# Performance work log

Hardware: AMD Instinct MI355X
Metric: run time of the kernel (lower is better)

Reference implementation:

```python
import jax, jax.numpy as jnp
import numpy as np

VOCAB = 50000
WORD_EMB = 300
N_QNODE = 3
N_KNODE = 3
HID = 512
N_OUT = 300
N_ANS = 32000
N_LAYERS = 3
MIN_NORM = 1e-15
EPS = 1e-7

# ---- Hyperboloid manifold ops (HGCN convention, curvature c, K = 1/c) ----

def proj_tan0(u):
    # zero out the time coordinate
    return u.at[..., :1].set(0.0)

def expmap0(u, c):
    K = 1.0 / c
    sqrtK = jnp.sqrt(K)
    d = u[..., 1:]
    n = jnp.clip(jnp.linalg.norm(d, axis=-1, keepdims=True), MIN_NORM, None)
    theta = n / sqrtK
    return jnp.concatenate([sqrtK * jnp.cosh(theta), sqrtK * jnp.sinh(theta) * d / n], axis=-1)

def logmap0(x, c):
    K = 1.0 / c
    sqrtK = jnp.sqrt(K)
    d = x[..., 1:]
    n = jnp.clip(jnp.linalg.norm(d, axis=-1, keepdims=True), MIN_NORM, None)
    theta = jnp.clip(x[..., :1] / sqrtK, 1.0 + EPS, None)
    rest = sqrtK * jnp.arccosh(theta) * d / n
    return jnp.concatenate([jnp.zeros_like(rest[..., :1]), rest], axis=-1)

def proj(x, c):
    K = 1.0 / c
    d = x[..., 1:]
    first = jnp.sqrt(jnp.clip(K + jnp.sum(d * d, axis=-1, keepdims=True), EPS, None))
    return jnp.concatenate([first, d], axis=-1)

def hyperbolic_emb(x, c):
    return proj(expmap0(proj_tan0(x), c), c)


def setup_inputs() -> dict:
    key = jax.random.key(0)
    ks = jax.random.split(key, 16)
    B, NQ, NK = 256, 30, 100
    inp = {}
    inp['he_ques_id'] = jax.random.randint(ks[0], (B, NQ, N_QNODE), 0, VOCAB)
    inp['he_kg_id'] = jax.random.randint(ks[1], (B, NK, N_KNODE), 0, VOCAB)
    inp['emb_table'] = jax.random.normal(ks[2], (VOCAB, WORD_EMB), jnp.float32)
    inp['q2h_w'] = jax.random.normal(ks[3], (WORD_EMB * N_QNODE, HID), jnp.float32) * 0.01
    inp['q2h_b'] = jnp.zeros((HID,), jnp.float32)
    inp['k2h_w'] = jax.random.normal(ks[4], (WORD_EMB * N_KNODE, HID), jnp.float32) * 0.01
    inp['k2h_b'] = jnp.zeros((HID,), jnp.float32)
    inp['Wk'] = jax.random.normal(ks[5], (N_LAYERS, HID, HID), jnp.float32) * 0.05
    inp['Wq'] = jax.random.normal(ks[6], (N_LAYERS, HID, HID), jnp.float32) * 0.05
    inp['curv'] = jnp.ones((N_LAYERS + 1,), jnp.float32)
    inp['proj1_w'] = jax.random.normal(ks[7], (2 * HID, HID), jnp.float32) * 0.02
    inp['proj1_b'] = jnp.zeros((HID,), jnp.float32)
    inp['proj2_w'] = jax.random.normal(ks[8], (HID, N_OUT), jnp.float32) * 0.02
    inp['proj2_b'] = jnp.zeros((N_OUT,), jnp.float32)
    inp['glove_cands'] = jax.random.normal(ks[9], (N_ANS, N_OUT), jnp.float32)
    return inp


def reference(he_ques_id, he_kg_id, emb_table, q2h_w, q2h_b, k2h_w, k2h_b,
              Wk, Wq, curv, proj1_w, proj1_b, proj2_w, proj2_b, glove_cands):
    B = he_ques_id.shape[0]
    c0 = curv[0]
    cL = curv[N_LAYERS]

    # embedding lookup + flatten hyperedge nodes
    he_q = emb_table[he_ques_id].reshape(B, he_ques_id.shape[1], -1)  # (B,Nq,900)
    he_k = emb_table[he_kg_id].reshape(B, he_kg_id.shape[1], -1)      # (B,Nk,900)
    he_q = jnp.where(jnp.isnan(he_q), 0.0, he_q)
    he_k = jnp.where(jnp.isnan(he_k), 0.0, he_k)

    he_q = he_q @ q2h_w + q2h_b   # (B,Nq,H)
    he_k = he_k @ k2h_w + k2h_b   # (B,Nk,H)

    q = hyperbolic_emb(he_q, c0)  # (B,Nq,H) on hyperboloid
    k = hyperbolic_emb(he_k, c0)  # (B,Nk,H)

    scale = 1.0 / np.sqrt(HID)
    for i in range(N_LAYERS):
        c_in, c_out = curv[i], curv[i + 1]
        kt = proj_tan0(logmap0(k, c_in))
        qt = proj_tan0(logmap0(q, c_in))
        kp = kt @ Wk[i]
        qp = qt @ Wq[i]
        s = jnp.einsum('bkh,bqh->bkq', kp, qp) * scale
        att_k = jnp.einsum('bkq,bqh->bkh', jax.nn.softmax(s, axis=-1), qt) + kt
        att_q = jnp.einsum('bqk,bkh->bqh', jax.nn.softmax(jnp.swapaxes(s, 1, 2), axis=-1), kt) + qt
        k = proj(expmap0(proj_tan0(att_k), c_out), c_out)
        q = proj(expmap0(proj_tan0(att_q), c_out), c_out)

    # mean pool over hyperedges, concat kg||ques
    last_kq = jnp.concatenate([k.mean(axis=1), q.mean(axis=1)], axis=1)  # (B,2H)
    euc = proj_tan0(logmap0(last_kq, cL))
    h = jax.nn.relu(euc @ proj1_w + proj1_b)
    out = h @ proj2_w + proj2_b               # (B,300)
    sim = out @ glove_cands.T                 # (B,32000)
    pred = jax.nn.log_softmax(sim, axis=1)
    return pred
```

## Files before the change

### kernel.cpp

```cpp
#include <hip/hip_runtime.h>
#include <math.h>

#define BATCH 256
#define NQ 30
#define NK 100
#define HID 512
#define WORD 300
#define KIN 900
#define KP 928
#define NANS 32000
#define NOUT 300
#define NOUTP 384
#define NTG 12
#define NLAYERS 3
#define MQT (BATCH * NQ)
#define MKT (BATCH * NK)
#define SCALE 0.044194173824159216f
#define KTLD 520
#define CLDST 136

typedef __attribute__((ext_vector_type(8))) short bf16x8;
typedef __attribute__((ext_vector_type(4))) float f32x4;
typedef unsigned short ushort_t;

__device__ __forceinline__ unsigned short f2bf(float f) {
  unsigned int u = __float_as_uint(f);
  u = (u + 0x7FFF + ((u >> 16) & 1)) >> 16;
  return (unsigned short)u;
}
__device__ __forceinline__ float bf2f(unsigned short s) {
  return __uint_as_float(((unsigned int)s) << 16);
}

typedef const __attribute__((address_space(1))) unsigned int* gas_u32;
typedef __attribute__((address_space(3))) unsigned int* las_u32;
__device__ __forceinline__ void gld_lds16(const void* g, void* l) {
  __builtin_amdgcn_global_load_lds((gas_u32)g, (las_u32)l, 16, 0, 0);
}

__device__ __forceinline__ int xcd_swz_linear() {
  const int nwg = gridDim.x * gridDim.y;
  const int orig = blockIdx.y * gridDim.x + blockIdx.x;
  const int q = nwg >> 3, r = nwg & 7;
  const int xcd = orig & 7, idx = orig >> 3;
  return (xcd < r ? xcd * (q + 1) : r * (q + 1) + (xcd - r) * q) + idx;
}

__device__ __forceinline__ float waveReduceSum(float v) {
#pragma unroll
  for (int o = 32; o > 0; o >>= 1) v += __shfl_xor(v, o);
  return v;
}
__device__ float blockReduceSum512(float v) {
  __shared__ float sm[8];
  int lane = threadIdx.x & 63, w = threadIdx.x >> 6;
  v = waveReduceSum(v);
  if (lane == 0) sm[w] = v;
  __syncthreads();
  float r = 0.f;
#pragma unroll
  for (int i = 0; i < 8; ++i) r += sm[i];
  __syncthreads();
  return r;
}

template <int SWZB, int BIAS, int OUTF32, int OUTBF16, int ZC0, int RELU>
__global__ __launch_bounds__(256) void mfma_gemm2(
    const ushort_t* __restrict__ A1, const ushort_t* __restrict__ Bt1,
    const float* __restrict__ bias1, float* __restrict__ C1,
    ushort_t* __restrict__ Cb1, int M1b,
    const ushort_t* __restrict__ A2, const ushort_t* __restrict__ Bt2,
    const float* __restrict__ bias2, float* __restrict__ C2,
    ushort_t* __restrict__ Cb2,
    size_t zsA, size_t zsB, size_t zsC,
    int N, int K, int nbias) {
  __shared__ __align__(16) ushort_t smem[128 * CLDST];
  const int wg = xcd_swz_linear();
  const int bx = wg % gridDim.x, by = wg / gridDim.x;
  const int z = blockIdx.z;
  const bool sel = (by >= M1b);
  const ushort_t* A = (sel ? A2 : A1) + z * zsA;
  const ushort_t* Bt = (sel ? Bt2 : Bt1) + z * zsB;
  const float* bias = sel ? bias2 : bias1;
  float* C = (sel ? C2 : C1);
  ushort_t* Cb = (sel ? Cb2 : Cb1);
  if (C) C += z * zsC;
  if (Cb) Cb += z * zsC;
  const int row0 = (sel ? (by - M1b) : by) * 128;
  const int col0 = bx * 128;

  const int tid = threadIdx.x;
  const int lane = tid & 63, w = tid >> 6;
  const int wr = w >> 1, wc = w & 1;
  const int s_r = lane & 15, s_kq = lane >> 4;
  const int nt = K / 32;

  const size_t a_src0 = (size_t)(row0 + (w * 2 + 0) * 16 + s_r) * K + s_kq * 8;
  const size_t a_src1 = (size_t)(row0 + (w * 2 + 1) * 16 + s_r) * K + s_kq * 8;
  const size_t b_lin0 = (size_t)(col0 + (w * 2 + 0) * 16 + s_r) * K + s_kq * 8;
  const size_t b_lin1 = (size_t)(col0 + (w * 2 + 1) * 16 + s_r) * K + s_kq * 8;
  const size_t b_swz0 = ((size_t)(col0 >> 7) * nt) * 4096 + (w * 2 + 0) * 512 + lane * 8;
  const size_t b_swz1 = b_swz0 + 512;

  auto stageAB = [&](int t, int bsel) {
    const int k0 = t * 32;
    ushort_t* Ab = smem + bsel * 4096;
    ushort_t* Bb = smem + 8192 + bsel * 4096;
    gld_lds16(A + a_src0 + k0, Ab + (w * 2 + 0) * 512);
    gld_lds16(A + a_src1 + k0, Ab + (w * 2 + 1) * 512);
    if (SWZB) {
      gld_lds16(Bt + b_swz0 + (size_t)t * 4096, Bb + (w * 2 + 0) * 512);
      gld_lds16(Bt + b_swz1 + (size_t)t * 4096, Bb + (w * 2 + 1) * 512);
    } else {
      gld_lds16(Bt + b_lin0 + k0, Bb + (w * 2 + 0) * 512);
      gld_lds16(Bt + b_lin1 + k0, Bb + (w * 2 + 1) * 512);
    }
  };

  f32x4 acc[4][4];
#pragma unroll
  for (int i = 0; i < 4; ++i)
#pragma unroll
    for (int j = 0; j < 4; ++j) acc[i][j] = (f32x4){0.f, 0.f, 0.f, 0.f};

  stageAB(0, 0);
  __syncthreads();
  for (int t = 0; t < nt; ++t) {
    const int cur = t & 1;
    if (t + 1 < nt) stageAB(t + 1, cur ^ 1);
    const ushort_t* Ab = smem + cur * 4096;
    const ushort_t* Bb = smem + 8192 + cur * 4096;
    bf16x8 af[4], bfr[4];
#pragma unroll
    for (int mi = 0; mi < 4; ++mi)
      af[mi] = *(const bf16x8*)(Ab + (wr * 4 + mi) * 512 + lane * 8);
#pragma unroll
    for (int nj = 0; nj < 4; ++nj)
      bfr[nj] = *(const bf16x8*)(Bb + (wc * 4 + nj) * 512 + lane * 8);
#pragma unroll
    for (int mi = 0; mi < 4; ++mi)
#pragma unroll
      for (int nj = 0; nj < 4; ++nj)
        acc[mi][nj] = __builtin_amdgcn_mfma_f32_16x16x32_bf16(
            af[mi], bfr[nj], acc[mi][nj], 0, 0, 0);
    __syncthreads();
  }

  if (OUTBF16) {
#pragma unroll
    for (int nj = 0; nj < 4; ++nj) {
      const int nl = wc * 64 + nj * 16 + (lane & 15);
      const int n = col0 + nl;
      const float bb = BIAS ? ((n < nbias) ? bias[n] : 0.f) : 0.f;
#pragma unroll
      for (int mi = 0; mi < 4; ++mi) {
        f32x4 v = acc[mi][nj];
#pragma unroll
        for (int r = 0; r < 4; ++r) {
          const int ml = wr * 64 + mi * 16 + (lane >> 4) * 4 + r;
          float val = v[r] + bb;
          if (RELU) val = fmaxf(val, 0.f);
          if (ZC0 && n == 0) val = 0.f;
          smem[ml * CLDST + nl] = f2bf(val);
        }
      }
    }
    __syncthreads();
#pragma unroll
    for (int j = 0; j < 8; ++j) {
      const int e = j * 2048 + tid * 8;
      const int ml = e >> 7, nl = e & 127;
      uint4 v = *(const uint4*)(smem + ml * CLDST + nl);
      *(uint4*)(Cb + (size_t)(row0 + ml) * N + col0 + nl) = v;
    }
  }
  if (OUTF32) {
#pragma unroll
    for (int nj = 0; nj < 4; ++nj) {
      const int n = col0 + wc * 64 + nj * 16 + (lane & 15);
      const float bb = BIAS ? ((n < nbias) ? bias[n] : 0.f) : 0.f;
#pragma unroll
      for (int mi = 0; mi < 4; ++mi) {
        f32x4 v = acc[mi][nj];
#pragma unroll
        for (int r = 0; r < 4; ++r) {
          const int m = row0 + wr * 64 + mi * 16 + (lane >> 4) * 4 + r;
          float val = v[r] + bb;
          if (RELU) val = fmaxf(val, 0.f);
          if (ZC0 && n == 0) val = 0.f;
          C[(size_t)m * N + n] = val;
        }
      }
    }
  }
}

__global__ __launch_bounds__(256) void gather_all_k(
    const int* __restrict__ qid, const int* __restrict__ kid,
    const float* __restrict__ emb, ushort_t* __restrict__ gq,
    ushort_t* __restrict__ gk) {
  int m = blockIdx.x;
  const int* ids;
  ushort_t* outp;
  if (m < MQT) {
    ids = qid + m * 3;
    outp = gq + (size_t)m * KP;
  } else {
    m -= MQT;
    ids = kid + m * 3;
    outp = gk + (size_t)m * KP;
  }
  const int t = threadIdx.x;
  if (t >= KP / 4) return;
  const int k = t * 4;
  ushort4 o = make_ushort4(0, 0, 0, 0);
  if (k < KIN) {
    const int node = (k >= 600) ? 2 : ((k >= 300) ? 1 : 0);
    const int off = k - node * 300;
    const int id = ids[node];
    float4 v = *(const float4*)(emb + (size_t)id * 300 + off);
    if (v.x != v.x) v.x = 0.f;
    if (v.y != v.y) v.y = 0.f;
    if (v.z != v.z) v.z = 0.f;
    if (v.w != v.w) v.w = 0.f;
    o = make_ushort4(f2bf(v.x), f2bf(v.y), f2bf(v.z), f2bf(v.w));
  }
  *(ushort4*)(outp + k) = o;
}

__global__ __launch_bounds__(256) void tcast4_k(
    const float* __restrict__ q2h_w, const float* __restrict__ k2h_w,
    const float* __restrict__ p1w, const float* __restrict__ p2w,
    ushort_t* __restrict__ q2h_wt, ushort_t* __restrict__ k2h_wt,
    ushort_t* __restrict__ p1wt, ushort_t* __restrict__ p2wt) {
  const int z = blockIdx.z;
  const float* src;
  ushort_t* dst;
  int R, Cc, Rp, Cp;
  if (z == 0)      { src = q2h_w; dst = q2h_wt; R = KIN;  Cc = HID;  Rp = KP;   Cp = HID; }
  else if (z == 1) { src = k2h_w; dst = k2h_wt; R = KIN;  Cc = HID;  Rp = KP;   Cp = HID; }
  else if (z == 2) { src = p1w; dst = p1wt; R = 1024; Cc = HID;  Rp = 1024; Cp = HID; }
  else             { src = p2w; dst = p2wt; R = HID;  Cc = NOUT; Rp = HID;  Cp = NOUTP; }
  const int r0 = blockIdx.y * 32, c0 = blockIdx.x * 32;
  if (r0 >= Rp || c0 >= Cp) return;
  __shared__ float t[32][33];
  const int tx = threadIdx.x & 31, ty = threadIdx.x >> 5;
#pragma unroll
  for (int i = 0; i < 4; ++i) {
    int r = r0 + ty + i * 8, c = c0 + tx;
    t[ty + i * 8][tx] = (r < R && c < Cc) ? src[(size_t)r * Cc + c] : 0.f;
  }
  __syncthreads();
#pragma unroll
  for (int i = 0; i < 4; ++i) {
    int c = c0 + ty + i * 8, r = r0 + tx;
    if (c < Cp && r < Rp) dst[(size_t)c * Rp + r] = f2bf(t[tx][ty + i * 8]);
  }
}

__global__ __launch_bounds__(256) void gcast_swz_k(
    const float* __restrict__ glove, ushort_t* __restrict__ gs) {
  const int ts = blockIdx.x, gp = blockIdx.y;
  ushort_t* dst = gs + ((size_t)gp * NTG + ts) * 4096;
  for (int g = threadIdx.x; g < 512; g += 256) {
    const int o = g * 8;
    const int chunk = o >> 9, kq = (o >> 7) & 3, rl = (o >> 3) & 15;
    const int row = gp * 128 + chunk * 16 + rl;
    const int kb = ts * 32 + kq * 8;
    ushort_t tmp[8];
    if (kb + 8 <= NOUT) {
      const float* s = glove + (size_t)row * NOUT + kb;
      float2 a0 = *(const float2*)(s + 0);
      float2 a1 = *(const float2*)(s + 2);
      float2 a2 = *(const float2*)(s + 4);
      float2 a3 = *(const float2*)(s + 6);
      tmp[0] = f2bf(a0.x); tmp[1] = f2bf(a0.y);
      tmp[2] = f2bf(a1.x); tmp[3] = f2bf(a1.y);
      tmp[4] = f2bf(a2.x); tmp[5] = f2bf(a2.y);
      tmp[6] = f2bf(a3.x); tmp[7] = f2bf(a3.y);
    } else {
#pragma unroll
      for (int j = 0; j < 8; ++j) {
        const int k = kb + j;
        tmp[j] = (k < NOUT) ? f2bf(glove[(size_t)row * NOUT + k]) : (ushort_t)0;
      }
    }
    *(ushort4*)(dst + o) = make_ushort4(tmp[0], tmp[1], tmp[2], tmp[3]);
    *(ushort4*)(dst + o + 4) = make_ushort4(tmp[4], tmp[5], tmp[6], tmp[7]);
  }
}

__global__ __launch_bounds__(128) void castrows_k(
    const float* __restrict__ Wk, const float* __restrict__ Wq,
    ushort_t* __restrict__ Wkr, ushort_t* __restrict__ Wqr) {
  const int idx = blockIdx.x;
  const int mat = idx >> 9, row = idx & 511;
  const float* src = (mat < 3 ? Wk + (size_t)mat * HID * HID
                              : Wq + (size_t)(mat - 3) * HID * HID) + (size_t)row * HID;
  ushort_t* dst = (mat < 3 ? Wkr + (size_t)mat * HID * HID
                           : Wqr + (size_t)(mat - 3) * HID * HID) + (size_t)row * HID;
  const int k = threadIdx.x * 4;
  float4 v = *(const float4*)(src + k);
  *(ushort4*)(dst + k) = make_ushort4(f2bf(v.x), f2bf(v.y), f2bf(v.z), f2bf(v.w));
}

__global__ __launch_bounds__(512) void att_fused_k(
    const ushort_t* __restrict__ Qp, const ushort_t* __restrict__ Ktc,
    const ushort_t* __restrict__ Qc, ushort_t* __restrict__ Kn,
    ushort_t* __restrict__ Qn) {
  const int b = blockIdx.x;
  __shared__ float S_lds[NK][32];
  __shared__ float PqT[NK][32];
  __shared__ __align__(16) ushort_t kts[NK * KTLD];
  __shared__ __align__(16) ushort_t qts[NQ * HID];
  const int tid = threadIdx.x;
  const int w = tid >> 6, lane = tid & 63;
  const ushort_t* ktg = Ktc + (size_t)b * NK * HID;
  const ushort_t* qtg = Qc + (size_t)b * NQ * HID;

  for (int e = tid; e < NK * 64; e += 512) {
    const int r = e >> 6, c16 = e & 63;
    gld_lds16(ktg + (size_t)r * HID + c16 * 8, kts + (size_t)r * KTLD + c16 * 8);
  }
  for (int e = tid; e < NQ * 64; e += 512) {
    const int r = e >> 6, c16 = e & 63;
    gld_lds16(qtg + (size_t)r * HID + c16 * 8, qts + (size_t)r * HID + c16 * 8);
  }
  __syncthreads();

  if (w < 7) {
    const int r = lane & 15, kq = lane >> 4;
    const ushort_t* qpb = Qp + (size_t)b * NQ * HID;
    const int rowA = w * 16 + r;
    const int rowA_c = (rowA < NK) ? rowA : (NK - 1);
    const int qr1 = (16 + r) < NQ ? (16 + r) : NQ - 1;
    f32x4 a0 = {0.f, 0.f, 0.f, 0.f}, a1 = {0.f, 0.f, 0.f, 0.f};
    for (int k0 = 0; k0 < HID; k0 += 32) {
      bf16x8 af = *(const bf16x8*)(kts + (size_t)rowA_c * KTLD + k0 + kq * 8);
      bf16x8 b0 = *(const bf16x8*)(qpb + (size_t)r * HID + k0 + kq * 8);
      bf16x8 b1 = *(const bf16x8*)(qpb + (size_t)qr1 * HID + k0 + kq * 8);
      a0 = __builtin_amdgcn_mfma_f32_16x16x32_bf16(af, b0, a0, 0, 0, 0);
      a1 = __builtin_amdgcn_mfma_f32_16x16x32_bf16(af, b1, a1, 0, 0, 0);
    }
    const int q0 = lane & 15, mb = (lane >> 4) * 4;
#pragma unroll
    for (int rr = 0; rr < 4; ++rr) {
      const int mA = w * 16 + mb + rr;
      if (mA < NK) {
        S_lds[mA][q0] = a0[rr] * SCALE;
        if (q0 + 16 < NQ) S_lds[mA][q0 + 16] = a1[rr] * SCALE;
      }
    }
  }
  __syncthreads();
  if (tid < NQ) {
    const int q = tid;
    float m = -1e30f;
    for (int kr = 0; kr < NK; ++kr) m = fmaxf(m, S_lds[kr][q]);
    float s = 0.f;
    for (int kr = 0; kr < NK; ++kr) {
      float e = expf(S_lds[kr][q] - m);
      PqT[kr][q] = e;
      s += e;
    }
    float inv = 1.f / s;
    for (int kr = 0; kr < NK; ++kr) PqT[kr][q] *= inv;
  } else if (tid >= 32 && tid < 32 + NK) {
    const int kr = tid - 32;
    PqT[kr][30] = 0.f;
    PqT[kr][31] = 0.f;
  }
  __syncthreads();
  if (tid < NK) {
    const int kr = tid;
    float m = -1e30f;
#pragma unroll
    for (int q = 0; q < NQ; ++q) m = fmaxf(m, S_lds[kr][q]);
    float s = 0.f;
    float e[NQ];
#pragma unroll
    for (int q = 0; q < NQ; ++q) {
      e[q] = expf(S_lds[kr][q] - m);
      s += e[q];
    }
    float inv = 1.f / s;
#pragma unroll
    for (int q = 0; q < NQ; ++q) S_lds[kr][q] = e[q] * inv;
    S_lds[kr][30] = 0.f;
    S_lds[kr][31] = 0.f;
  }
  __syncthreads();

  const int c = tid;
  float qx[32], ax[32];
#pragma unroll
  for (int q = 0; q < NQ; ++q) qx[q] = bf2f(qts[q * HID + c]);
  qx[30] = 0.f;
  qx[31] = 0.f;
#pragma unroll
  for (int i = 0; i < 32; ++i) ax[i] = 0.f;
  ushort_t* kout = Kn + (size_t)b * NK * HID;
  for (int kr = 0; kr < NK; ++kr) {
    const float kx = bf2f(kts[(size_t)kr * KTLD + c]);
    float sx = kx;
#pragma unroll
    for (int g = 0; g < 8; ++g) {
      float4 pk = *(const float4*)&S_lds[kr][g * 4];
      sx = fmaf(pk.x, qx[g * 4 + 0], sx);
      sx = fmaf(pk.y, qx[g * 4 + 1], sx);
      sx = fmaf(pk.z, qx[g * 4 + 2], sx);
      sx = fmaf(pk.w, qx[g * 4 + 3], sx);
      float4 pq = *(const float4*)&PqT[kr][g * 4];
      ax[g * 4 + 0] = fmaf(pq.x, kx, ax[g * 4 + 0]);
      ax[g * 4 + 1] = fmaf(pq.y, kx, ax[g * 4 + 1]);
      ax[g * 4 + 2] = fmaf(pq.z, kx, ax[g * 4 + 2]);
      ax[g * 4 + 3] = fmaf(pq.w, kx, ax[g * 4 + 3]);
    }
    kout[(size_t)kr * HID + c] = f2bf(sx);
  }
  ushort_t* qout = Qn + (size_t)b * NQ * HID;
#pragma unroll
  for (int q = 0; q < NQ; ++q)
    qout[(size_t)q * HID + c] = f2bf(ax[q] + qx[q]);
}

__global__ __launch_bounds__(512) void finale_k(
    const ushort_t* __restrict__ Kb, const ushort_t* __restrict__ Qb,
    ushort_t* __restrict__ lastb, const float* __restrict__ curv) {
  const int b = blockIdx.x, tid = threadIdx.x;
  const int w = tid >> 6, lane = tid & 63;
  const float c = curv[NLAYERS];
  const float Kc = 1.f / c, sqrtK = sqrtf(Kc);
  __shared__ float fsc[NK + NQ];
  __shared__ float fst[NK + NQ];
  const ushort_t* xkp = Kb + (size_t)b * NK * HID;
  const ushort_t* xqp = Qb + (size_t)b * NQ * HID;

  for (int r = w; r < NK + NQ; r += 8) {
    const ushort_t* row =
        (r < NK) ? (xkp + (size_t)r * HID) : (xqp + (size_t)(r - NK) * HID);
    bf16x8 v = *(const bf16x8*)(row + lane * 8);
    float ss = 0.f;
#pragma unroll
    for (int j = 0; j < 8; ++j) {
      float t = bf2f((unsigned short)v[j]);
      ss = fmaf(t, t, ss);
    }
    ss = waveReduceSum(ss);
    if (lane == 0) {
      float n = fmaxf(sqrtf(ss), 1e-15f);
      float f = sqrtK * sinhf(n / sqrtK) / n;
      fsc[r] = f;
      fst[r] = sqrtf(fmaxf(Kc + f * f * ss, 1e-7f));
    }
  }
  __syncthreads();

  float mk, mq;
  if (tid == 0) {
    float sk = 0.f, sq2 = 0.f;
    for (int r = 0; r < NK; ++r) sk += fst[r];
    for (int r = 0; r < NQ; ++r) sq2 += fst[NK + r];
    mk = sk;
    mq = sq2;
  } else {
    float sk = 0.f, sq2 = 0.f;
    for (int r = 0; r < NK; ++r)
      sk = fmaf(fsc[r], bf2f(xkp[(size_t)r * HID + tid]), sk);
    for (int r = 0; r < NQ; ++r)
      sq2 = fmaf(fsc[NK + r], bf2f(xqp[(size_t)r * HID + tid]), sq2);
    mk = sk;
    mq = sq2;
  }
  mk *= (1.f / NK);
  mq *= (1.f / NQ);

  float sq = ((tid == 0) ? 0.f : mk * mk) + mq * mq;
  float ssall = blockReduceSum512(sq);
  __shared__ float x0sh;
  if (tid == 0) x0sh = mk;
  __syncthreads();
  const float x0 = x0sh;
  const float n = fmaxf(sqrtf(ssall), 1e-15f);
  const float theta = fmaxf(x0 / sqrtK, 1.f + 1e-7f);
  const float rr = sqrtK * acoshf(theta) / n;
  ushort_t* ob = lastb + (size_t)b * 1024;
  ob[tid] = (tid == 0) ? (ushort_t)0 : f2bf(rr * mk);
  ob[512 + tid] = f2bf(rr * mq);
}

__global__ __launch_bounds__(512) void logsoftmax_k(float* __restrict__ x) {
  const int b = blockIdx.x, tid = threadIdx.x;
  float4* row = (float4*)(x + (size_t)b * NANS);
  float m = -3.4e38f, s = 0.f;
  for (int i = tid; i < NANS / 4; i += 512) {
    float4 v = row[i];
    float lm = fmaxf(fmaxf(v.x, v.y), fmaxf(v.z, v.w));
    float nm = fmaxf(m, lm);
    s = s * expf(m - nm) + expf(v.x - nm) + expf(v.y - nm) +
        expf(v.z - nm) + expf(v.w - nm);
    m = nm;
  }
#pragma unroll
  for (int o = 32; o > 0; o >>= 1) {
    float mo = __shfl_xor(m, o);
    float so = __shfl_xor(s, o);
    float nm = fmaxf(m, mo);
    s = s * expf(m - nm) + so * expf(mo - nm);
    m = nm;
  }
  __shared__ float smm[8], sms[8];
  const int w = tid >> 6, lane = tid & 63;
  if (lane == 0) { smm[w] = m; sms[w] = s; }
  __syncthreads();
  float gm = smm[0], gs = sms[0];
#pragma unroll
  for (int i = 1; i < 8; ++i) {
    float nm = fmaxf(gm, smm[i]);
    gs = gs * expf(gm - nm) + sms[i] * expf(smm[i] - nm);
    gm = nm;
  }
  const float lse = gm + logf(gs);
  for (int i = tid; i < NANS / 4; i += 512) {
    float4 v = row[i];
    v.x -= lse; v.y -= lse; v.z -= lse; v.w -= lse;
    row[i] = v;
  }
}

extern "C" void kernel_launch(void* const* d_in, const int* in_sizes, int n_in,
                              void* d_out, int out_size, void* d_ws, size_t ws_size,
                              hipStream_t stream) {
  const int* qid = (const int*)d_in[0];
  const int* kid = (const int*)d_in[1];
  const float* emb = (const float*)d_in[2];
  const float* q2h_w = (const float*)d_in[3];
  const float* q2h_b = (const float*)d_in[4];
  const float* k2h_w = (const float*)d_in[5];
  const float* k2h_b = (const float*)d_in[6];
  const float* Wk = (const float*)d_in[7];
  const float* Wq = (const float*)d_in[8];
  const float* curv = (const float*)d_in[9];
  const float* p1w = (const float*)d_in[10];
  const float* p1b = (const float*)d_in[11];
  const float* p2w = (const float*)d_in[12];
  const float* p2b = (const float*)d_in[13];
  const float* glove = (const float*)d_in[14];
  float* out = (float*)d_out;

  ushort_t* u = (ushort_t*)d_ws;
  ushort_t* Ks0 = u;
  ushort_t* Ks1 = Ks0 + (size_t)MKT * HID;
  ushort_t* Qs0 = Ks1 + (size_t)MKT * HID;
  ushort_t* Qs1 = Qs0 + (size_t)MQT * HID;
  ushort_t* Qps = Qs1 + (size_t)MQT * HID;
  ushort_t* gq = Qps + (size_t)MQT * HID;
  ushort_t* gk = gq + (size_t)MQT * KP;
  ushort_t* q2h_wt = gk + (size_t)MKT * KP;
  ushort_t* k2h_wt = q2h_wt + (size_t)HID * KP;
  ushort_t* Wkr = k2h_wt + (size_t)HID * KP;
  ushort_t* Wqr = Wkr + (size_t)NLAYERS * HID * HID;
  ushort_t* Mb = Wqr + (size_t)NLAYERS * HID * HID;
  ushort_t* p1wt = Mb + (size_t)NLAYERS * HID * HID;
  ushort_t* p2wt = p1wt + (size_t)HID * 1024;
  ushort_t* lastb = p2wt + (size_t)NOUTP * HID;
  ushort_t* h1b = lastb + (size_t)BATCH * 1024;
  ushort_t* o2b = h1b + (size_t)BATCH * HID;
  ushort_t* gsw = o2b + (size_t)BATCH * NOUTP;

  gather_all_k<<<MQT + MKT, 256, 0, stream>>>(qid, kid, emb, gq, gk);
  tcast4_k<<<dim3(16, 32, 4), 256, 0, stream>>>(
      q2h_w, k2h_w, p1w, p2w, q2h_wt, k2h_wt, p1wt, p2wt);
  castrows_k<<<6 * HID, 128, 0, stream>>>(Wk, Wq, Wkr, Wqr);
  gcast_swz_k<<<dim3(NTG, 250), 256, 0, stream>>>(glove, gsw);

  mfma_gemm2<0, 0, 0, 1, 0, 0><<<dim3(HID / 128, HID / 128, NLAYERS), 256, 0, stream>>>(
      Wkr, Wqr, nullptr, nullptr, Mb, HID / 128,
      Wkr, Wqr, nullptr, nullptr, Mb,
      (size_t)HID * HID, (size_t)HID * HID, (size_t)HID * HID, HID, HID, HID);

  mfma_gemm2<0, 1, 0, 1, 1, 0><<<dim3(HID / 128, MQT / 128 + MKT / 128), 256, 0, stream>>>(
      gq, q2h_wt, q2h_b, nullptr, Qs0, MQT / 128,
      gk, k2h_wt, k2h_b, nullptr, Ks0, 0, 0, 0, HID, KP, HID);

  ushort_t* Kc = Ks0;
  ushort_t* Kn = Ks1;
  ushort_t* Qc = Qs0;
  ushort_t* Qn = Qs1;
  for (int i = 0; i < NLAYERS; ++i) {
    mfma_gemm2<0, 0, 0, 1, 0, 0><<<dim3(HID / 128, MQT / 128), 256, 0, stream>>>(
        Qc, Mb + (size_t)i * HID * HID, nullptr, nullptr, Qps, MQT / 128,
        Qc, Mb + (size_t)i * HID * HID, nullptr, nullptr, Qps,
        0, 0, 0, HID, HID, HID);
    att_fused_k<<<BATCH, 512, 0, stream>>>(Qps, Kc, Qc, Kn, Qn);
    ushort_t* t1 = Kc; Kc = Kn; Kn = t1;
    ushort_t* t2 = Qc; Qc = Qn; Qn = t2;
  }

  finale_k<<<BATCH, 512, 0, stream>>>(Kc, Qc, lastb, curv);

  mfma_gemm2<0, 1, 0, 1, 0, 1><<<dim3(HID / 128, BATCH / 128), 256, 0, stream>>>(
      lastb, p1wt, p1b, nullptr, h1b, BATCH / 128,
      lastb, p1wt, p1b, nullptr, h1b, 0, 0, 0, HID, 1024, HID);
  mfma_gemm2<0, 1, 0, 1, 0, 0><<<dim3(NOUTP / 128, BATCH / 128), 256, 0, stream>>>(
      h1b, p2wt, p2b, nullptr, o2b, BATCH / 128,
      h1b, p2wt, p2b, nullptr, o2b, 0, 0, 0, NOUTP, HID, NOUT);
  mfma_gemm2<1, 0, 1, 0, 0, 0><<<dim3(NANS / 128, BATCH / 128), 256, 0, stream>>>(
      o2b, gsw, nullptr, out, nullptr, BATCH / 128,
      o2b, gsw, nullptr, out, nullptr, 0, 0, 0, NANS, NOUTP, NANS);
  logsoftmax_k<<<BATCH, 512, 0, stream>>>(out);
}
```

Before: 445.9 us.

## Compute attention-weighted aggregations in att_fused_k with bf16 MFMA

Replaces the per-thread scalar FMA loops for the two attention products (P_k·Q and P_q^T·K) with 16x16x32 bf16 MFMA tiles. Softmax probabilities are now stored as bf16 in LDS, padded to K=32 or 128, and the S buffer gets a padded stride. The goal is to move the per-column scalar work and register-heavy accumulators onto matrix cores. In exchange it adds bf16 rounding of the probabilities, gathers of strided 2-byte elements from LDS to build the B fragments, and scattered 2-byte global stores.

```diff
diff --git a/kernel.cpp b/kernel.cpp
--- a/kernel.cpp
+++ b/kernel.cpp
@@ -18,6 +18,8 @@
 #define SCALE 0.044194173824159216f
 #define KTLD 520
 #define CLDST 136
+#define SST 36
+#define PQLD 136
 
 typedef __attribute__((ext_vector_type(8))) short bf16x8;
 typedef __attribute__((ext_vector_type(4))) float f32x4;
@@ -309,8 +311,8 @@
     const ushort_t* __restrict__ Qc, ushort_t* __restrict__ Kn,
     ushort_t* __restrict__ Qn) {
   const int b = blockIdx.x;
-  __shared__ float S_lds[NK][32];
-  __shared__ float PqT[NK][32];
+  __shared__ __align__(16) float S_lds[112 * SST];
+  __shared__ __align__(16) ushort_t Pq[32 * PQLD];
   __shared__ __align__(16) ushort_t kts[NK * KTLD];
   __shared__ __align__(16) ushort_t qts[NQ * HID];
   const int tid = threadIdx.x;
@@ -347,81 +349,133 @@
     for (int rr = 0; rr < 4; ++rr) {
       const int mA = w * 16 + mb + rr;
       if (mA < NK) {
-        S_lds[mA][q0] = a0[rr] * SCALE;
-        if (q0 + 16 < NQ) S_lds[mA][q0 + 16] = a1[rr] * SCALE;
-      }
-    }
-  }
-  __syncthreads();
+        S_lds[mA * SST + q0] = a0[rr] * SCALE;
+        if (q0 + 16 < NQ) S_lds[mA * SST + q0 + 16] = a1[rr] * SCALE;
+      }
+    }
+  }
+  __syncthreads();
+  float e2[NQ];
+  float inv2 = 0.f;
+  const int kr2 = tid - 32;
+  const bool do2b = (kr2 >= 0 && kr2 < NK);
   if (tid < NQ) {
     const int q = tid;
     float m = -1e30f;
-    for (int kr = 0; kr < NK; ++kr) m = fmaxf(m, S_lds[kr][q]);
+    for (int kr = 0; kr < NK; ++kr) m = fmaxf(m, S_lds[kr * SST + q]);
     float s = 0.f;
-    for (int kr = 0; kr < NK; ++kr) {
-      float e = expf(S_lds[kr][q] - m);
-      PqT[kr][q] = e;
-      s += e;
-    }
+    for (int kr = 0; kr < NK; ++kr) s += expf(S_lds[kr * SST + q] - m);
     float inv = 1.f / s;
-    for (int kr = 0; kr < NK; ++kr) PqT[kr][q] *= inv;
-  } else if (tid >= 32 && tid < 32 + NK) {
-    const int kr = tid - 32;
-    PqT[kr][30] = 0.f;
-    PqT[kr][31] = 0.f;
-  }
-  __syncthreads();
-  if (tid < NK) {
-    const int kr = tid;
+    for (int kr = 0; kr < NK; ++kr)
+      Pq[q * PQLD + kr] = f2bf(expf(S_lds[kr * SST + q] - m) * inv);
+    for (int kr = NK; kr < 128; ++kr) Pq[q * PQLD + kr] = 0;
+  } else if (tid < 32) {
+    for (int kr = 0; kr < 128; ++kr) Pq[tid * PQLD + kr] = 0;
+  } else if (do2b) {
     float m = -1e30f;
 #pragma unroll
-    for (int q = 0; q < NQ; ++q) m = fmaxf(m, S_lds[kr][q]);
+    for (int q = 0; q < NQ; ++q) m = fmaxf(m, S_lds[kr2 * SST + q]);
     float s = 0.f;
-    float e[NQ];
 #pragma unroll
     for (int q = 0; q < NQ; ++q) {
-      e[q] = expf(S_lds[kr][q] - m);
-      s += e[q];
-    }
-    float inv = 1.f / s;
-#pragma unroll
-    for (int q = 0; q < NQ; ++q) S_lds[kr][q] = e[q] * inv;
-    S_lds[kr][30] = 0.f;
-    S_lds[kr][31] = 0.f;
-  }
-  __syncthreads();
-
-  const int c = tid;
-  float qx[32], ax[32];
-#pragma unroll
-  for (int q = 0; q < NQ; ++q) qx[q] = bf2f(qts[q * HID + c]);
-  qx[30] = 0.f;
-  qx[31] = 0.f;
-#pragma unroll
-  for (int i = 0; i < 32; ++i) ax[i] = 0.f;
-  ushort_t* kout = Kn + (size_t)b * NK * HID;
-  for (int kr = 0; kr < NK; ++kr) {
-    const float kx = bf2f(kts[(size_t)kr * KTLD + c]);
-    float sx = kx;
-#pragma unroll
-    for (int g = 0; g < 8; ++g) {
-      float4 pk = *(const float4*)&S_lds[kr][g * 4];
-      sx = fmaf(pk.x, qx[g * 4 + 0], sx);
-      sx = fmaf(pk.y, qx[g * 4 + 1], sx);
-      sx = fmaf(pk.z, qx[g * 4 + 2], sx);
-      sx = fmaf(pk.w, qx[g * 4 + 3], sx);
-      float4 pq = *(const float4*)&PqT[kr][g * 4];
-      ax[g * 4 + 0] = fmaf(pq.x, kx, ax[g * 4 + 0]);
-      ax[g * 4 + 1] = fmaf(pq.y, kx, ax[g * 4 + 1]);
-      ax[g * 4 + 2] = fmaf(pq.z, kx, ax[g * 4 + 2]);
-      ax[g * 4 + 3] = fmaf(pq.w, kx, ax[g * 4 + 3]);
-    }
-    kout[(size_t)kr * HID + c] = f2bf(sx);
-  }
-  ushort_t* qout = Qn + (size_t)b * NQ * HID;
-#pragma unroll
-  for (int q = 0; q < NQ; ++q)
-    qout[(size_t)q * HID + c] = f2bf(ax[q] + qx[q]);
+      e2[q] = expf(S_lds[kr2 * SST + q] - m);
+      s += e2[q];
+    }
+    inv2 = 1.f / s;
+  }
+  __syncthreads();
+  ushort_t* Pk = (ushort_t*)S_lds;
+  if (do2b) {
+    ushort_t* prow = Pk + kr2 * 72;
+#pragma unroll
+    for (int q = 0; q < NQ; ++q) prow[q] = f2bf(e2[q] * inv2);
+    prow[30] = 0;
+    prow[31] = 0;
+  }
+  __syncthreads();
+
+  const int cl = lane & 15, g8 = (lane >> 4) * 8;
+  {
+    bf16x8 bk[4];
+#pragma unroll
+    for (int nt = 0; nt < 4; ++nt) {
+      const int col = w * 64 + nt * 16 + cl;
+      union { ushort_t u[8]; bf16x8 v; } pb;
+#pragma unroll
+      for (int j = 0; j < 8; ++j) {
+        const int q = g8 + j;
+        pb.u[j] = qts[(q < NQ ? q : NQ - 1) * HID + col];
+      }
+      bk[nt] = pb.v;
+    }
+    ushort_t* kout = Kn + (size_t)b * NK * HID;
+#pragma unroll
+    for (int mt = 0; mt < 7; ++mt) {
+      bf16x8 af = *(const bf16x8*)(Pk + (mt * 16 + cl) * 72 + g8);
+      f32x4 ac[4];
+#pragma unroll
+      for (int nt = 0; nt < 4; ++nt) {
+        ac[nt] = (f32x4){0.f, 0.f, 0.f, 0.f};
+        ac[nt] = __builtin_amdgcn_mfma_f32_16x16x32_bf16(af, bk[nt], ac[nt], 0, 0, 0);
+      }
+#pragma unroll
+      for (int nt = 0; nt < 4; ++nt) {
+        const int col = w * 64 + nt * 16 + cl;
+#pragma unroll
+        for (int r = 0; r < 4; ++r) {
+          const int row = mt * 16 + (lane >> 4) * 4 + r;
+          if (row < NK) {
+            float v = ac[nt][r] + bf2f(kts[(size_t)row * KTLD + col]);
+            kout[(size_t)row * HID + col] = f2bf(v);
+          }
+        }
+      }
+    }
+  }
+  {
+    f32x4 aq[2][4];
+#pragma unroll
+    for (int mt = 0; mt < 2; ++mt)
+#pragma unroll
+      for (int nt = 0; nt < 4; ++nt) aq[mt][nt] = (f32x4){0.f, 0.f, 0.f, 0.f};
+#pragma unroll
+    for (int ks = 0; ks < 4; ++ks) {
+      bf16x8 bq[4];
+#pragma unroll
+      for (int nt = 0; nt < 4; ++nt) {
+        const int col = w * 64 + nt * 16 + cl;
+        union { ushort_t u[8]; bf16x8 v; } pb;
+#pragma unroll
+        for (int j = 0; j < 8; ++j) {
+          const int kr = ks * 32 + g8 + j;
+          pb.u[j] = kts[(size_t)(kr < NK ? kr : NK - 1) * KTLD + col];
+        }
+        bq[nt] = pb.v;
+      }
+#pragma unroll
+      for (int mt = 0; mt < 2; ++mt) {
+        bf16x8 af = *(const bf16x8*)(Pq + (mt * 16 + cl) * PQLD + ks * 32 + g8);
+#pragma unroll
+        for (int nt = 0; nt < 4; ++nt)
+          aq[mt][nt] = __builtin_amdgcn_mfma_f32_16x16x32_bf16(af, bq[nt], aq[mt][nt], 0, 0, 0);
+      }
+    }
+    ushort_t* qout = Qn + (size_t)b * NQ * HID;
+#pragma unroll
+    for (int mt = 0; mt < 2; ++mt)
+#pragma unroll
+      for (int nt = 0; nt < 4; ++nt) {
+        const int col = w * 64 + nt * 16 + cl;
+#pragma unroll
+        for (int r = 0; r < 4; ++r) {
+          const int row = mt * 16 + (lane >> 4) * 4 + r;
+          if (row < NQ) {
+            float v = aq[mt][nt][r] + bf2f(qts[(size_t)row * HID + col]);
+            qout[(size_t)row * HID + col] = f2bf(v);
+          }
+        }
+      }
+  }
 }
 
 __global__ __launch_bounds__(512) void finale_k(
```

Measured after the change: 402.2 us. 1.11x faster.

## Split fused attention into score/softmax kernel plus batched MFMA P·V GEMMs

Applied to the files above, without the earlier changes.

The monolithic per-batch attention kernel, which did the two softmax-weighted sums with scalar FMAs, is replaced by three steps. A score+softmax kernel writes bf16 probability matrices Pk and Pq. Two batched MFMA GEMM launches then compute att_k and att_q with the residual add fused into the epilogue. The GEMM epilogue also writes transposed copies of K and Q (padded to 128 and 32 rows per batch) for the next layer's B operand, and Q storage is padded to 32 rows per batch. This adds launches and extra global traffic for the P matrices and transposed outputs, and pads the small per-batch GEMMs, which wastes MFMA work.

```diff
diff --git a/kernel.cpp b/kernel.cpp
--- a/kernel.cpp
+++ b/kernel.cpp
@@ -14,10 +14,11 @@
 #define NTG 12
 #define NLAYERS 3
 #define MQT (BATCH * NQ)
+#define MQ32 (BATCH * 32)
 #define MKT (BATCH * NK)
 #define SCALE 0.044194173824159216f
-#define KTLD 520
 #define CLDST 136
+#define SST 36
 
 typedef __attribute__((ext_vector_type(8))) short bf16x8;
 typedef __attribute__((ext_vector_type(4))) float f32x4;
@@ -51,6 +52,11 @@
   for (int o = 32; o > 0; o >>= 1) v += __shfl_xor(v, o);
   return v;
 }
+__device__ __forceinline__ float waveReduceMax(float v) {
+#pragma unroll
+  for (int o = 32; o > 0; o >>= 1) v = fmaxf(v, __shfl_xor(v, o));
+  return v;
+}
 __device__ float blockReduceSum512(float v) {
   __shared__ float sm[8];
   int lane = threadIdx.x & 63, w = threadIdx.x >> 6;
@@ -64,16 +70,19 @@
   return r;
 }
 
-template <int SWZB, int BIAS, int OUTF32, int OUTBF16, int ZC0, int RELU>
+template <int SWZB, int BIAS, int OUTF32, int OUTBF16, int ZC0, int RELU,
+          int RESID, int TRANS>
 __global__ __launch_bounds__(256) void mfma_gemm2(
     const ushort_t* __restrict__ A1, const ushort_t* __restrict__ Bt1,
     const float* __restrict__ bias1, float* __restrict__ C1,
-    ushort_t* __restrict__ Cb1, int M1b,
+    ushort_t* __restrict__ Cb1, const ushort_t* __restrict__ R1,
+    ushort_t* __restrict__ TB1, int pb1, int pbt1, size_t zsT1, int M1b,
     const ushort_t* __restrict__ A2, const ushort_t* __restrict__ Bt2,
     const float* __restrict__ bias2, float* __restrict__ C2,
-    ushort_t* __restrict__ Cb2,
+    ushort_t* __restrict__ Cb2, const ushort_t* __restrict__ R2,
+    ushort_t* __restrict__ TB2, int pb2, int pbt2, size_t zsT2,
     size_t zsA, size_t zsB, size_t zsC,
-    int N, int K, int nbias) {
+    int N, int K, int nbias, int mv) {
   __shared__ __align__(16) ushort_t smem[128 * CLDST];
   const int wg = xcd_swz_linear();
   const int bx = wg % gridDim.x, by = wg / gridDim.x;
@@ -84,8 +93,14 @@
   const float* bias = sel ? bias2 : bias1;
   float* C = (sel ? C2 : C1);
   ushort_t* Cb = (sel ? Cb2 : Cb1);
+  const ushort_t* R = (sel ? R2 : R1);
+  ushort_t* TB = (sel ? TB2 : TB1);
+  const int pb = sel ? pb2 : pb1;
+  const int pbt = sel ? pbt2 : pbt1;
+  const size_t zsT = sel ? zsT2 : zsT1;
   if (C) C += z * zsC;
   if (Cb) Cb += z * zsC;
+  if (RESID && R) R += z * zsC;
   const int row0 = (sel ? (by - M1b) : by) * 128;
   const int col0 = bx * 128;
 
@@ -161,6 +176,7 @@
           float val = v[r] + bb;
           if (RELU) val = fmaxf(val, 0.f);
           if (ZC0 && n == 0) val = 0.f;
+          if (RESID) val += bf2f(R[(size_t)(row0 + ml) * N + n]);
           smem[ml * CLDST + nl] = f2bf(val);
         }
       }
@@ -170,8 +186,38 @@
     for (int j = 0; j < 8; ++j) {
       const int e = j * 2048 + tid * 8;
       const int ml = e >> 7, nl = e & 127;
-      uint4 v = *(const uint4*)(smem + ml * CLDST + nl);
-      *(uint4*)(Cb + (size_t)(row0 + ml) * N + col0 + nl) = v;
+      if (ml < mv) {
+        uint4 v = *(const uint4*)(smem + ml * CLDST + nl);
+        *(uint4*)(Cb + (size_t)(row0 + ml) * N + col0 + nl) = v;
+      }
+    }
+    if (TRANS) {
+      const int colL = tid & 127;
+#pragma unroll
+      for (int t2 = 0; t2 < 8; ++t2) {
+        const int grp = (tid >> 7) + t2 * 2;
+        const int mlb = grp * 8;
+        const int grow = row0 + mlb;
+        const int b2 = grow / pb;
+        const int r = grow - b2 * pb;
+        if (r >= pbt) continue;
+        union { ushort_t u[8]; uint4 v; ushort4 h[2]; } pk;
+#pragma unroll
+        for (int j = 0; j < 8; ++j) pk.u[j] = smem[(mlb + j) * CLDST + colL];
+        ushort_t* tb = TB + (size_t)(z + b2) * zsT + (size_t)(col0 + colL) * pbt;
+        if (r + 8 <= pb) {
+          if ((r & 7) == 0) {
+            *(uint4*)(tb + r) = pk.v;
+          } else {
+            *(ushort4*)(tb + r) = pk.h[0];
+            *(ushort4*)(tb + r + 4) = pk.h[1];
+          }
+        } else {
+          *(ushort4*)(tb + r) = pk.h[0];
+          ushort_t* tb2 = TB + (size_t)(z + b2 + 1) * zsT + (size_t)(col0 + colL) * pbt;
+          *(ushort4*)tb2 = pk.h[1];
+        }
+      }
     }
   }
   if (OUTF32) {
@@ -195,6 +241,69 @@
   }
 }
 
+__global__ __launch_bounds__(512) void s_softmax_k(
+    const ushort_t* __restrict__ Kc, const ushort_t* __restrict__ Qps,
+    ushort_t* __restrict__ Pk, ushort_t* __restrict__ Pq) {
+  const int b = blockIdx.x;
+  __shared__ __align__(16) float S_lds[112 * SST];
+  const int tid = threadIdx.x;
+  const int w = tid >> 6, lane = tid & 63;
+  if (w < 7) {
+    const int r = lane & 15, kq = lane >> 4;
+    const ushort_t* ktb = Kc + (size_t)b * NK * HID;
+    const ushort_t* qpb = Qps + (size_t)b * 32 * HID;
+    const int rowA = w * 16 + r;
+    const int rowA_c = (rowA < NK) ? rowA : (NK - 1);
+    const int qr1 = (16 + r) < NQ ? (16 + r) : NQ - 1;
+    f32x4 a0 = {0.f, 0.f, 0.f, 0.f}, a1 = {0.f, 0.f, 0.f, 0.f};
+    for (int k0 = 0; k0 < HID; k0 += 32) {
+      bf16x8 af = *(const bf16x8*)(ktb + (size_t)rowA_c * HID + k0 + kq * 8);
+      bf16x8 b0 = *(const bf16x8*)(qpb + (size_t)r * HID + k0 + kq * 8);
+      bf16x8 b1 = *(const bf16x8*)(qpb + (size_t)qr1 * HID + k0 + kq * 8);
+      a0 = __builtin_amdgcn_mfma_f32_16x16x32_bf16(af, b0, a0, 0, 0, 0);
+      a1 = __builtin_amdgcn_mfma_f32_16x16x32_bf16(af, b1, a1, 0, 0, 0);
+    }
+    const int q0 = lane & 15, mb = (lane >> 4) * 4;
+#pragma unroll
+    for (int rr = 0; rr < 4; ++rr) {
+      const int mA = w * 16 + mb + rr;
+      S_lds[mA * SST + q0] = a0[rr] * SCALE;
+      if (q0 + 16 < NQ) S_lds[mA * SST + q0 + 16] = a1[rr] * SCALE;
+    }
+  }
+  __syncthreads();
+  if (tid < NQ) {
+    const int q = tid;
+    float m = -1e30f;
+    for (int kr = 0; kr < NK; ++kr) m = fmaxf(m, S_lds[kr * SST + q]);
+    float s = 0.f;
+    for (int kr = 0; kr < NK; ++kr) s += expf(S_lds[kr * SST + q] - m);
+    float inv = 1.f / s;
+    ushort_t* pq = Pq + (size_t)b * 128 * 128 + q * 128;
+    for (int kr = 0; kr < NK; ++kr)
+      pq[kr] = f2bf(expf(S_lds[kr * SST + q] - m) * inv);
+    for (int kr = NK; kr < 128; ++kr) pq[kr] = 0;
+  } else if (tid >= 32 && tid < 32 + NK) {
+    const int kr = tid - 32;
+    float m = -1e30f;
+#pragma unroll
+    for (int q = 0; q < NQ; ++q) m = fmaxf(m, S_lds[kr * SST + q]);
+    float s = 0.f;
+    float e[NQ];
+#pragma unroll
+    for (int q = 0; q < NQ; ++q) {
+      e[q] = expf(S_lds[kr * SST + q] - m);
+      s += e[q];
+    }
+    float inv = 1.f / s;
+    ushort_t* pk = Pk + (size_t)b * 128 * 32 + kr * 32;
+#pragma unroll
+    for (int q = 0; q < NQ; ++q) pk[q] = f2bf(e[q] * inv);
+    pk[30] = 0;
+    pk[31] = 0;
+  }
+}
+
 __global__ __launch_bounds__(256) void gather_all_k(
     const int* __restrict__ qid, const int* __restrict__ kid,
     const float* __restrict__ emb, ushort_t* __restrict__ gq,
@@ -203,8 +312,9 @@
   const int* ids;
   ushort_t* outp;
   if (m < MQT) {
+    const int bb = m / 30, slot = m - bb * 30;
     ids = qid + m * 3;
-    outp = gq + (size_t)m * KP;
+    outp = gq + ((size_t)bb * 32 + slot) * KP;
   } else {
     m -= MQT;
     ids = kid + m * 3;
@@ -304,126 +414,6 @@
   *(ushort4*)(dst + k) = make_ushort4(f2bf(v.x), f2bf(v.y), f2bf(v.z), f2bf(v.w));
 }
 
-__global__ __launch_bounds__(512) void att_fused_k(
-    const ushort_t* __restrict__ Qp, const ushort_t* __restrict__ Ktc,
-    const ushort_t* __restrict__ Qc, ushort_t* __restrict__ Kn,
-    ushort_t* __restrict__ Qn) {
-  const int b = blockIdx.x;
-  __shared__ float S_lds[NK][32];
-  __shared__ float PqT[NK][32];
-  __shared__ __align__(16) ushort_t kts[NK * KTLD];
-  __shared__ __align__(16) ushort_t qts[NQ * HID];
-  const int tid = threadIdx.x;
-  const int w = tid >> 6, lane = tid & 63;
-  const ushort_t* ktg = Ktc + (size_t)b * NK * HID;
-  const ushort_t* qtg = Qc + (size_t)b * NQ * HID;
-
-  for (int e = tid; e < NK * 64; e += 512) {
-    const int r = e >> 6, c16 = e & 63;
-    gld_lds16(ktg + (size_t)r * HID + c16 * 8, kts + (size_t)r * KTLD + c16 * 8);
-  }
-  for (int e = tid; e < NQ * 64; e += 512) {
-    const int r = e >> 6, c16 = e & 63;
-    gld_lds16(qtg + (size_t)r * HID + c16 * 8, qts + (size_t)r * HID + c16 * 8);
-  }
-  __syncthreads();
-
-  if (w < 7) {
-    const int r = lane & 15, kq = lane >> 4;
-    const ushort_t* qpb = Qp + (size_t)b * NQ * HID;
-    const int rowA = w * 16 + r;
-    const int rowA_c = (rowA < NK) ? rowA : (NK - 1);
-    const int qr1 = (16 + r) < NQ ? (16 + r) : NQ - 1;
-    f32x4 a0 = {0.f, 0.f, 0.f, 0.f}, a1 = {0.f, 0.f, 0.f, 0.f};
-    for (int k0 = 0; k0 < HID; k0 += 32) {
-      bf16x8 af = *(const bf16x8*)(kts + (size_t)rowA_c * KTLD + k0 + kq * 8);
-      bf16x8 b0 = *(const bf16x8*)(qpb + (size_t)r * HID + k0 + kq * 8);
-      bf16x8 b1 = *(const bf16x8*)(qpb + (size_t)qr1 * HID + k0 + kq * 8);
-      a0 = __builtin_amdgcn_mfma_f32_16x16x32_bf16(af, b0, a0, 0, 0, 0);
-      a1 = __builtin_amdgcn_mfma_f32_16x16x32_bf16(af, b1, a1, 0, 0, 0);
-    }
-    const int q0 = lane & 15, mb = (lane >> 4) * 4;
-#pragma unroll
-    for (int rr = 0; rr < 4; ++rr) {
-      const int mA = w * 16 + mb + rr;
-      if (mA < NK) {
-        S_lds[mA][q0] = a0[rr] * SCALE;
-        if (q0 + 16 < NQ) S_lds[mA][q0 + 16] = a1[rr] * SCALE;
-      }
-    }
-  }
-  __syncthreads();
-  if (tid < NQ) {
-    const int q = tid;
-    float m = -1e30f;
-    for (int kr = 0; kr < NK; ++kr) m = fmaxf(m, S_lds[kr][q]);
-    float s = 0.f;
-    for (int kr = 0; kr < NK; ++kr) {
-      float e = expf(S_lds[kr][q] - m);
-      PqT[kr][q] = e;
-      s += e;
-    }
-    float inv = 1.f / s;
-    for (int kr = 0; kr < NK; ++kr) PqT[kr][q] *= inv;
-  } else if (tid >= 32 && tid < 32 + NK) {
-    const int kr = tid - 32;
-    PqT[kr][30] = 0.f;
-    PqT[kr][31] = 0.f;
-  }
-  __syncthreads();
-  if (tid < NK) {
-    const int kr = tid;
-    float m = -1e30f;
-#pragma unroll
-    for (int q = 0; q < NQ; ++q) m = fmaxf(m, S_lds[kr][q]);
-    float s = 0.f;
-    float e[NQ];
-#pragma unroll
-    for (int q = 0; q < NQ; ++q) {
-      e[q] = expf(S_lds[kr][q] - m);
-      s += e[q];
-    }
-    float inv = 1.f / s;
-#pragma unroll
-    for (int q = 0; q < NQ; ++q) S_lds[kr][q] = e[q] * inv;
-    S_lds[kr][30] = 0.f;
-    S_lds[kr][31] = 0.f;
-  }
-  __syncthreads();
-
-  const int c = tid;
-  float qx[32], ax[32];
-#pragma unroll
-  for (int q = 0; q < NQ; ++q) qx[q] = bf2f(qts[q * HID + c]);
-  qx[30] = 0.f;
-  qx[31] = 0.f;
-#pragma unroll
-  for (int i = 0; i < 32; ++i) ax[i] = 0.f;
-  ushort_t* kout = Kn + (size_t)b * NK * HID;
-  for (int kr = 0; kr < NK; ++kr) {
-    const float kx = bf2f(kts[(size_t)kr * KTLD + c]);
-    float sx = kx;
-#pragma unroll
-    for (int g = 0; g < 8; ++g) {
-      float4 pk = *(const float4*)&S_lds[kr][g * 4];
-      sx = fmaf(pk.x, qx[g * 4 + 0], sx);
-      sx = fmaf(pk.y, qx[g * 4 + 1], sx);
-      sx = fmaf(pk.z, qx[g * 4 + 2], sx);
-      sx = fmaf(pk.w, qx[g * 4 + 3], sx);
-      float4 pq = *(const float4*)&PqT[kr][g * 4];
-      ax[g * 4 + 0] = fmaf(pq.x, kx, ax[g * 4 + 0]);
-      ax[g * 4 + 1] = fmaf(pq.y, kx, ax[g * 4 + 1]);
-      ax[g * 4 + 2] = fmaf(pq.z, kx, ax[g * 4 + 2]);
-      ax[g * 4 + 3] = fmaf(pq.w, kx, ax[g * 4 + 3]);
-    }
-    kout[(size_t)kr * HID + c] = f2bf(sx);
-  }
-  ushort_t* qout = Qn + (size_t)b * NQ * HID;
-#pragma unroll
-  for (int q = 0; q < NQ; ++q)
-    qout[(size_t)q * HID + c] = f2bf(ax[q] + qx[q]);
-}
-
 __global__ __launch_bounds__(512) void finale_k(
     const ushort_t* __restrict__ Kb, const ushort_t* __restrict__ Qb,
     ushort_t* __restrict__ lastb, const float* __restrict__ curv) {
@@ -434,7 +424,7 @@
   __shared__ float fsc[NK + NQ];
   __shared__ float fst[NK + NQ];
   const ushort_t* xkp = Kb + (size_t)b * NK * HID;
-  const ushort_t* xqp = Qb + (size_t)b * NQ * HID;
+  const ushort_t* xqp = Qb + (size_t)b * 32 * HID;
 
   for (int r = w; r < NK + NQ; r += 8) {
     const ushort_t* row =
@@ -551,11 +541,17 @@
   ushort_t* u = (ushort_t*)d_ws;
   ushort_t* Ks0 = u;
   ushort_t* Ks1 = Ks0 + (size_t)MKT * HID;
-  ushort_t* Qs0 = Ks1 + (size_t)MKT * HID;
-  ushort_t* Qs1 = Qs0 + (size_t)MQT * HID;
-  ushort_t* Qps = Qs1 + (size_t)MQT * HID;
-  ushort_t* gq = Qps + (size_t)MQT * HID;
-  ushort_t* gk = gq + (size_t)MQT * KP;
+  ushort_t* KsT0 = Ks1 + (size_t)MKT * HID;
+  ushort_t* KsT1 = KsT0 + (size_t)BATCH * HID * 128;
+  ushort_t* Qs0 = KsT1 + (size_t)BATCH * HID * 128;
+  ushort_t* Qs1 = Qs0 + (size_t)MQ32 * HID;
+  ushort_t* QsT0 = Qs1 + (size_t)MQ32 * HID;
+  ushort_t* QsT1 = QsT0 + (size_t)BATCH * HID * 32;
+  ushort_t* Qps = QsT1 + (size_t)BATCH * HID * 32;
+  ushort_t* Pk = Qps + (size_t)MQ32 * HID;
+  ushort_t* Pq = Pk + (size_t)BATCH * 128 * 32;
+  ushort_t* gq = Pq + (size_t)BATCH * 128 * 128;
+  ushort_t* gk = gq + (size_t)MQ32 * KP;
   ushort_t* q2h_wt = gk + (size_t)MKT * KP;
   ushort_t* k2h_wt = q2h_wt + (size_t)HID * KP;
   ushort_t* Wkr = k2h_wt + (size_t)HID * KP;
@@ -574,39 +570,53 @@
   castrows_k<<<6 * HID, 128, 0, stream>>>(Wk, Wq, Wkr, Wqr);
   gcast_swz_k<<<dim3(NTG, 250), 256, 0, stream>>>(glove, gsw);
 
-  mfma_gemm2<0, 0, 0, 1, 0, 0><<<dim3(HID / 128, HID / 128, NLAYERS), 256, 0, stream>>>(
-      Wkr, Wqr, nullptr, nullptr, Mb, HID / 128,
-      Wkr, Wqr, nullptr, nullptr, Mb,
-      (size_t)HID * HID, (size_t)HID * HID, (size_t)HID * HID, HID, HID, HID);
-
-  mfma_gemm2<0, 1, 0, 1, 1, 0><<<dim3(HID / 128, MQT / 128 + MKT / 128), 256, 0, stream>>>(
-      gq, q2h_wt, q2h_b, nullptr, Qs0, MQT / 128,
-      gk, k2h_wt, k2h_b, nullptr, Ks0, 0, 0, 0, HID, KP, HID);
-
-  ushort_t* Kc = Ks0;
-  ushort_t* Kn = Ks1;
-  ushort_t* Qc = Qs0;
-  ushort_t* Qn = Qs1;
+  mfma_gemm2<0, 0, 0, 1, 0, 0, 0, 0><<<dim3(HID / 128, HID / 128, NLAYERS), 256, 0, stream>>>(
+      Wkr, Wqr, nullptr, nullptr, Mb, nullptr, nullptr, 128, 128, 0, HID / 128,
+      Wkr, Wqr, nullptr, nullptr, Mb, nullptr, nullptr, 128, 128, 0,
+      (size_t)HID * HID, (size_t)HID * HID, (size_t)HID * HID, HID, HID, HID, 128);
+
+  mfma_gemm2<0, 1, 0, 1, 1, 0, 0, 1><<<dim3(HID / 128, MQ32 / 128 + MKT / 128), 256, 0, stream>>>(
+      gq, q2h_wt, q2h_b, nullptr, Qs0, nullptr, QsT0, 32, 32, (size_t)HID * 32, MQ32 / 128,
+      gk, k2h_wt, k2h_b, nullptr, Ks0, nullptr, KsT0, 100, 128, (size_t)HID * 128,
+      0, 0, 0, HID, KP, HID, 128);
+
+  ushort_t *Kc = Ks0, *Kn = Ks1, *KcT = KsT0, *KnT = KsT1;
+  ushort_t *Qc = Qs0, *Qn = Qs1, *QcT = QsT0, *QnT = QsT1;
   for (int i = 0; i < NLAYERS; ++i) {
-    mfma_gemm2<0, 0, 0, 1, 0, 0><<<dim3(HID / 128, MQT / 128), 256, 0, stream>>>(
-        Qc, Mb + (size_t)i * HID * HID, nullptr, nullptr, Qps, MQT / 128,
-        Qc, Mb + (size_t)i * HID * HID, nullptr, nullptr, Qps,
-        0, 0, 0, HID, HID, HID);
-    att_fused_k<<<BATCH, 512, 0, stream>>>(Qps, Kc, Qc, Kn, Qn);
-    ushort_t* t1 = Kc; Kc = Kn; Kn = t1;
-    ushort_t* t2 = Qc; Qc = Qn; Qn = t2;
+    mfma_gemm2<0, 0, 0, 1, 0, 0, 0, 0><<<dim3(HID / 128, MQ32 / 128), 256, 0, stream>>>(
+        Qc, Mb + (size_t)i * HID * HID, nullptr, nullptr, Qps, nullptr, nullptr,
+        128, 128, 0, MQ32 / 128,
+        Qc, Mb + (size_t)i * HID * HID, nullptr, nullptr, Qps, nullptr, nullptr,
+        128, 128, 0, 0, 0, 0, HID, HID, HID, 128);
+    s_softmax_k<<<BATCH, 512, 0, stream>>>(Kc, Qps, Pk, Pq);
+    mfma_gemm2<0, 0, 0, 1, 0, 0, 1, 1><<<dim3(HID / 128, 1, BATCH), 256, 0, stream>>>(
+        Pk, QcT, nullptr, nullptr, Kn, Kc, KnT, 128, 128, (size_t)HID * 128, 1,
+        Pk, QcT, nullptr, nullptr, Kn, Kc, KnT, 128, 128, (size_t)HID * 128,
+        (size_t)128 * 32, (size_t)HID * 32, (size_t)NK * HID, HID, 32, HID, 100);
+    mfma_gemm2<0, 0, 0, 1, 0, 0, 1, 1><<<dim3(HID / 128, 1, BATCH), 256, 0, stream>>>(
+        Pq, KcT, nullptr, nullptr, Qn, Qc, QnT, 128, 32, (size_t)HID * 32, 1,
+        Pq, KcT, nullptr, nullptr, Qn, Qc, QnT, 128, 32, (size_t)HID * 32,
+        (size_t)128 * 128, (size_t)HID * 128, (size_t)32 * HID, HID, 128, HID, 32);
+    ushort_t* t;
+    t = Kc; Kc = Kn; Kn = t;
+    t = KcT; KcT = KnT; KnT = t;
+    t = Qc; Qc = Qn; Qn = t;
+    t = QcT; QcT = QnT; QnT = t;
   }
 
   finale_k<<<BATCH, 512, 0, stream>>>(Kc, Qc, lastb, curv);
 
-  mfma_gemm2<0, 1, 0, 1, 0, 1><<<dim3(HID / 128, BATCH / 128), 256, 0, stream>>>(
-      lastb, p1wt, p1b, nullptr, h1b, BATCH / 128,
-      lastb, p1wt, p1b, nullptr, h1b, 0, 0, 0, HID, 1024, HID);
-  mfma_gemm2<0, 1, 0, 1, 0, 0><<<dim3(NOUTP / 128, BATCH / 128), 256, 0, stream>>>(
-      h1b, p2wt, p2b, nullptr, o2b, BATCH / 128,
-      h1b, p2wt, p2b, nullptr, o2b, 0, 0, 0, NOUTP, HID, NOUT);
-  mfma_gemm2<1, 0, 1, 0, 0, 0><<<dim3(NANS / 128, BATCH / 128), 256, 0, stream>>>(
-      o2b, gsw, nullptr, out, nullptr, BATCH / 128,
-      o2b, gsw, nullptr, out, nullptr, 0, 0, 0, NANS, NOUTP, NANS);
+  mfma_gemm2<0, 1, 0, 1, 0, 1, 0, 0><<<dim3(HID / 128, BATCH / 128), 256, 0, stream>>>(
+      lastb, p1wt, p1b, nullptr, h1b, nullptr, nullptr, 128, 128, 0, BATCH / 128,
+      lastb, p1wt, p1b, nullptr, h1b, nullptr, nullptr, 128, 128, 0,
+      0, 0, 0, HID, 1024, HID, 128);
+  mfma_gemm2<0, 1, 0, 1, 0, 0, 0, 0><<<dim3(NOUTP / 128, BATCH / 128), 256, 0, stream>>>(
+      h1b, p2wt, p2b, nullptr, o2b, nullptr, nullptr, 128, 128, 0, BATCH / 128,
+      h1b, p2wt, p2b, nullptr, o2b, nullptr, nullptr, 128, 128, 0,
+      0, 0, 0, NOUTP, HID, NOUT, 128);
+  mfma_gemm2<1, 0, 1, 0, 0, 0, 0, 0><<<dim3(NANS / 128, BATCH / 128), 256, 0, stream>>>(
+      o2b, gsw, nullptr, out, nullptr, nullptr, nullptr, 128, 128, 0, BATCH / 128,
+      o2b, gsw, nullptr, out, nullptr, nullptr, nullptr, 128, 128, 0,
+      0, 0, 0, NANS, NOUTP, NANS, 128);
   logsoftmax_k<<<BATCH, 512, 0, stream>>>(out);
 }
```

After: 578.4 us. 29.7% more time.
